# Optimization experiments

Hardware: AMD Instinct MI355X
Metric: run time of the kernel (lower is better)

## Reference

```python
import jax, jax.numpy as jnp
import numpy as np

NUM_CLASSES = 2
IGNORE_INDEX = 0
B, H, W = 4, 512, 512
BIG_I = 2 ** 30  # int sentinel for 'no seed yet'
INF = jnp.float32(1e9)  # distance when a column/image has no seed


def _edt_to_seed(seed):
    """Exact 2D Euclidean distance transform: distance from every pixel to the
    nearest True pixel in `seed` [H, W] (matches scipy distance_transform_edt
    applied to an image whose zeros are `seed`).
    Pass 1: 1D nearest-seed distance down each column via cummax/cummin scans.
    Pass 2: exact lower envelope across rows by brute-force min over k:
            D^2(i,j) = min_k ( (j-k)^2 + g(i,k)^2 ).
    """
    h, w = seed.shape
    rows = jnp.arange(h, dtype=jnp.int32)[:, None]              # [H,1]
    last = jax.lax.cummax(jnp.where(seed, rows, -1), axis=0)     # last seed above
    d_fwd = jnp.where(last >= 0, rows - last, BIG_I)
    nxt = jax.lax.cummin(jnp.where(seed, rows, BIG_I), axis=0, reverse=True)
    d_bwd = jnp.where(nxt < BIG_I, nxt - rows, BIG_I)
    g = jnp.minimum(d_fwd, d_bwd)                                # [H,W] int
    g2 = jnp.where(g >= BIG_I // 2, INF * INF, (g * g).astype(jnp.float32))
    cols = jnp.arange(w, dtype=jnp.float32)
    sq = (cols[:, None] - cols[None, :]) ** 2                    # [Wj,Wk]
    d2 = jnp.min(g2[:, None, :] + sq[None, :, :], axis=-1)       # [H,Wj]
    return jnp.sqrt(d2)


def _distance_map_one(tgt):
    """tgt: [H, W] int labels -> [num_classes, H, W] signed distance maps."""
    maps = []
    for c in range(NUM_CLASSES):
        if c == IGNORE_INDEX:
            maps.append(jnp.zeros(tgt.shape, jnp.float32))
            continue
        mask = tgt == c
        pos_dist = _edt_to_seed(~mask)   # edt(posmask): dist to nearest background
        neg_dist = _edt_to_seed(mask)    # edt(negmask): dist to nearest foreground
        present = jnp.any(mask)          # 'if mask.sum() > 0' guard
        maps.append(jnp.where(present, neg_dist - pos_dist, 0.0))
    return jnp.stack(maps, axis=0)


def setup_inputs() -> dict:
    key = jax.random.key(0)
    k1, k2 = jax.random.split(key)
    pred = jax.random.normal(k1, (B, NUM_CLASSES, H, W), dtype=jnp.float32)
    target = jax.random.randint(k2, (B, H, W), 0, 2, dtype=jnp.int32)
    return {"pred": pred, "target": target}


def reference(pred, target):
    p = jax.nn.softmax(pred, axis=1)                         # [B,C,H,W]
    # sequential over batch to bound the [H,W,W] EDT intermediate
    dmaps = jax.lax.map(_distance_map_one, target)           # [B,C,H,W]
    return jnp.mean(p * dmaps)
```

## Files before the change

kernel.cpp:

```cpp
#include <hip/hip_runtime.h>
#include <math.h>

#define BB 4
#define HH 512
#define WW 512
#define HWSZ (HH * WW)
#define ROWS_BLOCKS 256

#define SK(x) ((x) + ((x) >> 5))


__global__ __launch_bounds__(64) void pack_kernel(
    const int* __restrict__ target,
    unsigned int* __restrict__ cw,
    int* __restrict__ flags,
    double* __restrict__ dacc,
    unsigned int* __restrict__ done)
{
    int gid = blockIdx.x * 64 + threadIdx.x;
    int b = gid >> 12;
    int rem = gid & 4095;
    int w = rem >> 8;
    int col = (rem & 255) << 1;

    if (gid == 0) { *dacc = 0.0; *done = 0u; }

    const int* t = target + b * HWSZ + (w << 5) * WW + col;
    unsigned int w0 = 0, w1 = 0;
#pragma unroll
    for (int i = 0; i < 32; ++i) {
        int2 v = *(const int2*)(t + i * WW);
        w0 |= (unsigned int)(v.x == 1) << i;
        w1 |= (unsigned int)(v.y == 1) << i;
    }
    ((uint2*)cw)[gid] = make_uint2(w0, w1);

    int cnt = __popc(w0) + __popc(w1);
#pragma unroll
    for (int off = 32; off > 0; off >>= 1) cnt += __shfl_down(cnt, off, 64);
    if (threadIdx.x == 0) flags[blockIdx.x] = (cnt > 0);
}

__global__ __launch_bounds__(512) void rows_kernel(
    const unsigned int* __restrict__ cw,
    const float* __restrict__ pred,
    const int* __restrict__ flags,
    double* __restrict__ dacc,
    unsigned int* __restrict__ done,
    float* __restrict__ out)
{
    __shared__ unsigned int sW[16 * 512];
    __shared__ float g2n[8][SK(511) + 1], g2p[8][SK(511) + 1];
    __shared__ float wsum[8];
    __shared__ int sPres;

    int blk = blockIdx.x;
    int b = blk >> 6;
    int g = blk & 63;
    int tid = threadIdx.x;
    int w = tid >> 6, lane = tid & 63;
    int row = 8 * g + w;
    int j0 = 8 * lane;

    const float* p0 = pred + (b * 2 + 0) * HWSZ + row * WW + j0;
    const float* p1 = pred + (b * 2 + 1) * HWSZ + row * WW + j0;
    float4 a0 = *(const float4*)(p0);
    float4 a1 = *(const float4*)(p0 + 4);
    float4 c0 = *(const float4*)(p1);
    float4 c1 = *(const float4*)(p1 + 4);

    if (w == 0) {
        int f = flags[b * 64 + lane];
        unsigned long long blt = __ballot(f != 0);
        if (lane == 0) sPres = (blt != 0ULL);
    }

    const uint4* cw4 = (const uint4*)(cw + b * 8192);
    uint4* sW4 = (uint4*)sW;
#pragma unroll
    for (int t = 0; t < 4; ++t)
        sW4[tid + 512 * t] = cw4[tid + 512 * t];
    __syncthreads();

    int wr = row >> 5, bit = row & 31;
    float* G2N = g2n[w];
    float* G2P = g2p[w];
    unsigned int loMask = 0xFFFFFFFFu >> (31 - bit);
    unsigned int hiMask = 0xFFFFFFFFu << bit;
#pragma unroll
    for (int t = 0; t < 8; ++t) {
        int col = lane + (t << 6);
        unsigned int Wr = sW[(wr << 9) + col];
        int dUp, dDn;
        unsigned int m = Wr & loMask;
        if (m) dUp = bit - (31 - __builtin_clz(m));
        else {
            dUp = 0x7FFFFFFF;
            for (int q = wr - 1; q >= 0; --q) {
                unsigned int W = sW[(q << 9) + col];
                if (W) { dUp = row - ((q << 5) + 31 - __builtin_clz(W)); break; }
            }
        }
        m = Wr & hiMask;
        if (m) dDn = __builtin_ctz(m) - bit;
        else {
            dDn = 0x7FFFFFFF;
            for (int q = wr + 1; q < 16; ++q) {
                unsigned int W = sW[(q << 9) + col];
                if (W) { dDn = (q << 5) + __builtin_ctz(W) - row; break; }
            }
        }
        int gN = min(dUp, dDn);
        G2N[SK(col)] = (gN > 511) ? 1e18f : (float)(gN * gN);
        unsigned int Vr = ~Wr;
        m = Vr & loMask;
        if (m) dUp = bit - (31 - __builtin_clz(m));
        else {
            dUp = 0x7FFFFFFF;
            for (int q = wr - 1; q >= 0; --q) {
                unsigned int W = ~sW[(q << 9) + col];
                if (W) { dUp = row - ((q << 5) + 31 - __builtin_clz(W)); break; }
            }
        }
        m = Vr & hiMask;
        if (m) dDn = __builtin_ctz(m) - bit;
        else {
            dDn = 0x7FFFFFFF;
            for (int q = wr + 1; q < 16; ++q) {
                unsigned int W = ~sW[(q << 9) + col];
                if (W) { dDn = (q << 5) + __builtin_ctz(W) - row; break; }
            }
        }
        int gP = min(dUp, dDn);
        G2P[SK(col)] = (gP > 511) ? 1e18f : (float)(gP * gP);
    }

    const float* sel[8];
    float bs[8], sgn[8];
#pragma unroll
    for (int jj = 0; jj < 8; ++jj) {
        float on = G2N[SK(j0 + jj)];
        float op = G2P[SK(j0 + jj)];
        bool fg = (on == 0.0f);
        sel[jj] = fg ? G2P : G2N;
        bs[jj]  = fg ? op : on;
        sgn[jj] = fg ? -1.0f : 1.0f;
    }
    for (int r = 1; r < WW; ++r) {
        float sq = (float)(r * r);
        float mx = 0.0f;
#pragma unroll
        for (int jj = 0; jj < 8; ++jj) mx = fmaxf(mx, bs[jj]);
        if (sq >= mx) break;
#pragma unroll
        for (int jj = 0; jj < 8; ++jj) {
            int kl = j0 + jj - r; kl = kl < 0 ? 0 : kl;
            int kr = j0 + jj + r; kr = kr > (WW - 1) ? (WW - 1) : kr;
            bs[jj] = fminf(bs[jj], sq + sel[jj][SK(kl)]);
            bs[jj] = fminf(bs[jj], sq + sel[jj][SK(kr)]);
        }
    }

    float x0[8] = {a0.x, a0.y, a0.z, a0.w, a1.x, a1.y, a1.z, a1.w};
    float x1[8] = {c0.x, c0.y, c0.z, c0.w, c1.x, c1.y, c1.z, c1.w};
    float acc = 0.0f;
#pragma unroll
    for (int jj = 0; jj < 8; ++jj) {
        float dist = sgn[jj] * sqrtf(bs[jj]);
        float prob = 1.0f / (1.0f + __expf(x0[jj] - x1[jj]));
        acc += prob * dist;
    }
#pragma unroll
    for (int off = 32; off > 0; off >>= 1) acc += __shfl_down(acc, off, 64);

    if (lane == 0) wsum[w] = acc;
    __syncthreads();
    if (tid == 0) {
        double s = 0.0;
#pragma unroll
        for (int i = 0; i < 8; ++i) s += (double)wsum[i];
        if (sPres) atomicAdd(dacc, s);
        __threadfence();
        unsigned int t = atomicAdd(done, 1u);
        if (t == ROWS_BLOCKS - 1) {
            double tot = atomicAdd(dacc, 0.0);
            out[0] = (float)(tot * (1.0 / 2097152.0));
        }
    }
}

extern "C" void kernel_launch(void* const* d_in, const int* in_sizes, int n_in,
                              void* d_out, int out_size, void* d_ws, size_t ws_size,
                              hipStream_t stream) {
    const float* pred = (const float*)d_in[0];
    const int* target = (const int*)d_in[1];
    float* out = (float*)d_out;

    char* ws = (char*)d_ws;
    int* flags = (int*)(ws + 0);
    double* dacc = (double*)(ws + 1024);
    unsigned int* done = (unsigned int*)(ws + 1032);
    unsigned int* cw = (unsigned int*)(ws + 32768);

    pack_kernel<<<256, 64, 0, stream>>>(target, cw, flags, dacc, done);
    rows_kernel<<<ROWS_BLOCKS, 512, 0, stream>>>(cw, pred, flags, dacc, done, out);
}
```

Measured before the change: 75.68 us.

## Fuse bit-packing into the distance kernel with per-batch spin barrier

```diff
diff --git a/kernel.cpp b/kernel.cpp
--- a/kernel.cpp
+++ b/kernel.cpp
@@ -5,54 +5,25 @@
 #define HH 512
 #define WW 512
 #define HWSZ (HH * WW)
-#define ROWS_BLOCKS 256
+#define NBLK 256
 
 #define SK(x) ((x) + ((x) >> 5))
 
 
-__global__ __launch_bounds__(64) void pack_kernel(
+__global__ __launch_bounds__(512) void fused_kernel(
     const int* __restrict__ target,
+    const float* __restrict__ pred,
     unsigned int* __restrict__ cw,
-    int* __restrict__ flags,
-    double* __restrict__ dacc,
-    unsigned int* __restrict__ done)
-{
-    int gid = blockIdx.x * 64 + threadIdx.x;
-    int b = gid >> 12;
-    int rem = gid & 4095;
-    int w = rem >> 8;
-    int col = (rem & 255) << 1;
-
-    if (gid == 0) { *dacc = 0.0; *done = 0u; }
-
-    const int* t = target + b * HWSZ + (w << 5) * WW + col;
-    unsigned int w0 = 0, w1 = 0;
-#pragma unroll
-    for (int i = 0; i < 32; ++i) {
-        int2 v = *(const int2*)(t + i * WW);
-        w0 |= (unsigned int)(v.x == 1) << i;
-        w1 |= (unsigned int)(v.y == 1) << i;
-    }
-    ((uint2*)cw)[gid] = make_uint2(w0, w1);
-
-    int cnt = __popc(w0) + __popc(w1);
-#pragma unroll
-    for (int off = 32; off > 0; off >>= 1) cnt += __shfl_down(cnt, off, 64);
-    if (threadIdx.x == 0) flags[blockIdx.x] = (cnt > 0);
-}
-
-__global__ __launch_bounds__(512) void rows_kernel(
-    const unsigned int* __restrict__ cw,
-    const float* __restrict__ pred,
-    const int* __restrict__ flags,
     double* __restrict__ dacc,
     unsigned int* __restrict__ done,
+    unsigned int* __restrict__ flagword,
+    unsigned int* __restrict__ pdone,
     float* __restrict__ out)
 {
     __shared__ unsigned int sW[16 * 512];
     __shared__ float g2n[8][SK(511) + 1], g2p[8][SK(511) + 1];
     __shared__ float wsum[8];
-    __shared__ int sPres;
+    __shared__ unsigned int sFW;
 
     int blk = blockIdx.x;
     int b = blk >> 6;
@@ -69,11 +40,31 @@
     float4 c0 = *(const float4*)(p1);
     float4 c1 = *(const float4*)(p1 + 4);
 
-    if (w == 0) {
-        int f = flags[b * 64 + lane];
-        unsigned long long blt = __ballot(f != 0);
-        if (lane == 0) sPres = (blt != 0ULL);
-    }
+    if (tid < 128) {
+        int idx = (g << 7) + tid;
+        int wr = idx >> 9;
+        int col = idx & 511;
+        const int* t = target + b * HWSZ + (wr << 5) * WW + col;
+        unsigned int word = 0;
+#pragma unroll
+        for (int i = 0; i < 32; ++i)
+            word |= (unsigned int)(t[i * WW] == 1) << i;
+        cw[b * 8192 + idx] = word;
+        int cnt = __popc(word);
+#pragma unroll
+        for (int off = 32; off > 0; off >>= 1) cnt += __shfl_down(cnt, off, 64);
+        if (lane == 0 && cnt > 0) atomicOr(flagword, 1u << b);
+    }
+    __syncthreads();
+    if (tid == 0) {
+        __threadfence();
+        atomicAdd(&pdone[b], 1u);
+        while (atomicAdd(&pdone[b], 0u) < 64u)
+            __builtin_amdgcn_s_sleep(2);
+        __threadfence();
+        sFW = atomicOr(flagword, 0u);
+    }
+    __syncthreads();
 
     const uint4* cw4 = (const uint4*)(cw + b * 8192);
     uint4* sW4 = (uint4*)sW;
@@ -179,10 +170,10 @@
         double s = 0.0;
 #pragma unroll
         for (int i = 0; i < 8; ++i) s += (double)wsum[i];
-        if (sPres) atomicAdd(dacc, s);
+        if ((sFW >> b) & 1u) atomicAdd(dacc, s);
         __threadfence();
         unsigned int t = atomicAdd(done, 1u);
-        if (t == ROWS_BLOCKS - 1) {
+        if (t == NBLK - 1) {
             double tot = atomicAdd(dacc, 0.0);
             out[0] = (float)(tot * (1.0 / 2097152.0));
         }
@@ -197,11 +188,13 @@
     float* out = (float*)d_out;
 
     char* ws = (char*)d_ws;
-    int* flags = (int*)(ws + 0);
-    double* dacc = (double*)(ws + 1024);
-    unsigned int* done = (unsigned int*)(ws + 1032);
+    double* dacc = (double*)(ws + 0);
+    unsigned int* done = (unsigned int*)(ws + 8);
+    unsigned int* flagword = (unsigned int*)(ws + 12);
+    unsigned int* pdone = (unsigned int*)(ws + 16);
     unsigned int* cw = (unsigned int*)(ws + 32768);
 
-    pack_kernel<<<256, 64, 0, stream>>>(target, cw, flags, dacc, done);
-    rows_kernel<<<ROWS_BLOCKS, 512, 0, stream>>>(cw, pred, flags, dacc, done, out);
+    hipMemsetAsync(ws, 0, 32, stream);
+    fused_kernel<<<NBLK, 512, 0, stream>>>(target, pred, cw, dacc, done,
+                                           flagword, pdone, out);
 }
```

Result: slower. 88.57 us (+17.0%).
